# Kernel optimization log

Hardware: AMD Instinct MI355X
Metric: run time of the kernel (lower is better)

The kernel has to match this reference:

```python
import jax, jax.numpy as jnp
import numpy as np


def _make_dplr_hippo(N):
    # Standard HiPPO-LegS -> NPLR -> DPLR construction (Annotated S4).
    p = np.sqrt(1.0 + 2.0 * np.arange(N))
    A = p[:, None] * p[None, :]
    A = np.tril(A) - np.diag(np.arange(N))
    A = -A
    P = np.sqrt(np.arange(N) + 0.5)
    B = np.sqrt(2.0 * np.arange(N) + 1.0)
    # Normal part S = A + P P^T is skew-symmetric + const*I
    S = A + P[:, None] * P[None, :]
    Lambda_real = np.mean(np.diagonal(S)) * np.ones(N)  # = -0.5
    Lambda_imag, V = np.linalg.eigh(S * -1j)            # S*-1j is Hermitian
    Lambda = Lambda_real + 1j * Lambda_imag
    Pc = V.conj().T @ P
    Bc = V.conj().T @ B
    return Lambda, Pc, Bc


N_STATE = 64
SEQ_LEN = 16384
BATCH = 1024


def setup_inputs() -> dict:
    key = jax.random.key(0)
    kx, kcr, kci = jax.random.split(key, 3)
    Lambda, P, B = _make_dplr_hippo(N_STATE)
    scale = 0.5 ** 0.5
    return {
        "x": jax.random.normal(kx, (BATCH, SEQ_LEN), dtype=jnp.float32),
        "Lambda_real": jnp.asarray(Lambda.real, dtype=jnp.float32),
        "Lambda_imag": jnp.asarray(Lambda.imag, dtype=jnp.float32),
        "P_real": jnp.asarray(P.real, dtype=jnp.float32),
        "P_imag": jnp.asarray(P.imag, dtype=jnp.float32),
        "B_real": jnp.asarray(B.real, dtype=jnp.float32),
        "B_imag": jnp.asarray(B.imag, dtype=jnp.float32),
        "C_real": jax.random.normal(kcr, (N_STATE,), dtype=jnp.float32) * scale,
        "C_imag": jax.random.normal(kci, (N_STATE,), dtype=jnp.float32) * scale,
        "step_size": jnp.asarray(0.01, dtype=jnp.float32),
    }


def _s4_fourier_kernel(Lambda, P, Q, B, C, step, L):
    # Evaluate the DPLR SSM generating function at the L roots of unity
    # via 4 Cauchy dot products (the classic S4 bottleneck).
    k = jnp.arange(L, dtype=jnp.float32)
    Omega = jnp.exp(-2j * jnp.pi * k / L)                 # [L] complex64
    g = (2.0 / step) * (1.0 - Omega) / (1.0 + Omega)      # [L]
    c = 2.0 / (1.0 + Omega)                               # [L]
    inv = 1.0 / (g[:, None] - Lambda[None, :])            # [L, N] Cauchy denominators
    a0 = jnp.conj(C)
    a1 = jnp.conj(Q)
    k00 = inv @ (a0 * B)   # [L]
    k01 = inv @ (a0 * P)
    k10 = inv @ (a1 * B)
    k11 = inv @ (a1 * P)
    return c * (k00 - k01 * (1.0 / (1.0 + k11)) * k10)    # [L]


def reference(x, Lambda_real, Lambda_imag, P_real, P_imag, B_real, B_imag,
              C_real, C_imag, step_size):
    L = x.shape[-1]
    Lambda = Lambda_real + 1j * Lambda_imag
    P = P_real + 1j * P_imag
    B = B_real + 1j * B_imag
    C_tilde = C_real + 1j * C_imag
    # Original computes the kernel under torch.no_grad().
    kernel = _s4_fourier_kernel(Lambda, P, P, B, C_tilde, step_size, L)  # [L]
    fft_u = jnp.fft.fft(x, n=L)              # [batch, L] complex64
    y = jnp.fft.ifft(kernel * fft_u, n=L)    # circular conv in freq domain
    return y.real
```

## Files before the change

kernel.cpp:

```cpp
#include <hip/hip_runtime.h>
#include <math.h>

#define LFFT 16384
#define NTHREADS 1024
#define LDS_PITCH 17

#define LDS_FENCE() asm volatile("s_waitcnt lgkmcnt(0)" ::: "memory")

__device__ __forceinline__ float2 cadd(float2 a, float2 b){ return make_float2(a.x+b.x, a.y+b.y); }
__device__ __forceinline__ float2 csub(float2 a, float2 b){ return make_float2(a.x-b.x, a.y-b.y); }
__device__ __forceinline__ float2 cmul(float2 a, float2 b){ return make_float2(a.x*b.x - a.y*b.y, a.x*b.y + a.y*b.x); }

template<int S> __device__ __forceinline__ float2 mul_is(float2 a) {
    return make_float2(-(float)S * a.y, (float)S * a.x);
}

template<int S> __device__ __forceinline__ void dft4_t(float2& a0, float2& a1, float2& a2, float2& a3) {
    float2 t0 = cadd(a0, a2);
    float2 t1 = csub(a0, a2);
    float2 t2 = cadd(a1, a3);
    float2 t3 = csub(a1, a3);
    a0 = cadd(t0, t2);
    a2 = csub(t0, t2);
    const float s = (float)S;
    a1 = make_float2(t1.x - s * t3.y, t1.y + s * t3.x);
    a3 = make_float2(t1.x + s * t3.y, t1.y - s * t3.x);
}

#define C16A 0.92387953251128675613f
#define C16B 0.70710678118654752440f
#define C16C 0.38268343236508977173f

template<int S> __device__ __forceinline__ void dft16_t(float2 r[16]) {
    const float s = (float)S;
    const float2 w1 = make_float2( C16A, s * C16C);
    const float2 w2 = make_float2( C16B, s * C16B);
    const float2 w3 = make_float2( C16C, s * C16A);
    const float2 w6 = make_float2(-C16B, s * C16B);
    const float2 w9 = make_float2(-C16A, -s * C16C);
    float2 g[4][4];
    #pragma unroll
    for (int b = 0; b < 4; ++b) {
        float2 a0 = r[b], a1 = r[b+4], a2 = r[b+8], a3 = r[b+12];
        dft4_t<S>(a0, a1, a2, a3);
        g[b][0] = a0; g[b][1] = a1; g[b][2] = a2; g[b][3] = a3;
    }
    g[1][1] = cmul(g[1][1], w1);  g[1][2] = cmul(g[1][2], w2);  g[1][3] = cmul(g[1][3], w3);
    g[2][1] = cmul(g[2][1], w2);  g[2][2] = mul_is<S>(g[2][2]); g[2][3] = cmul(g[2][3], w6);
    g[3][1] = cmul(g[3][1], w3);  g[3][2] = cmul(g[3][2], w6);  g[3][3] = cmul(g[3][3], w9);
    #pragma unroll
    for (int ka = 0; ka < 4; ++ka) {
        float2 a0 = g[0][ka], a1 = g[1][ka], a2 = g[2][ka], a3 = g[3][ka];
        dft4_t<S>(a0, a1, a2, a3);
        r[ka] = a0; r[ka+4] = a1; r[ka+8] = a2; r[ka+12] = a3;
    }
}

__device__ __forceinline__ void twiddle15(float2 r[16], float2 w) {
    float2 w2 = cmul(w, w);
    float2 we = w2;
    float2 wo = cmul(w, w2);
    r[1] = cmul(r[1], w);
    r[2] = cmul(r[2], we);
    r[3] = cmul(r[3], wo);
    #pragma unroll
    for (int j = 2; j <= 7; ++j) {
        we = cmul(we, w2);  r[2*j]   = cmul(r[2*j],   we);
        wo = cmul(wo, w2);  r[2*j+1] = cmul(r[2*j+1], wo);
    }
}

__global__ void s4_eval(const float* __restrict__ Lr, const float* __restrict__ Li,
                        const float* __restrict__ Pr, const float* __restrict__ Pi,
                        const float* __restrict__ Br, const float* __restrict__ Bi,
                        const float* __restrict__ Cr, const float* __restrict__ Ci,
                        const float* __restrict__ step_ptr,
                        float2* __restrict__ Kraw, float2* __restrict__ twid)
{
    int m = blockIdx.x * blockDim.x + threadIdx.x;
    if (m >= LFFT) return;
    double theta = (-2.0 * M_PI / (double)LFFT) * (double)m;
    double si, co;
    sincos(theta, &si, &co);
    twid[m] = make_float2((float)co, (float)si);

    double step = (double)step_ptr[0];
    double opr = 1.0 + co, opi = si;
    double omr = 1.0 - co, omi = -si;
    double iden = 1.0 / (opr*opr + opi*opi);
    double gs = 2.0 / step;
    double gr = gs * (omr*opr + omi*opi) * iden;
    double gi = gs * (omi*opr - omr*opi) * iden;
    double cr = 2.0 * opr * iden;
    double ci = -2.0 * opi * iden;

    double k00r=0,k00i=0,k01r=0,k01i=0,k10r=0,k10i=0,k11r=0,k11i=0;
    for (int n = 0; n < 64; ++n) {
        double dr = gr - (double)Lr[n];
        double di = gi - (double)Li[n];
        double id2 = 1.0 / (dr*dr + di*di);
        double vr =  dr * id2;
        double vi = -di * id2;
        double a0r = (double)Cr[n], a0i = -(double)Ci[n];
        double a1r = (double)Pr[n], a1i = -(double)Pi[n];
        double br  = (double)Br[n], bi  = (double)Bi[n];
        double pr  = (double)Pr[n], pi  = (double)Pi[n];
        double e00r = a0r*br - a0i*bi, e00i = a0r*bi + a0i*br;
        double e01r = a0r*pr - a0i*pi, e01i = a0r*pi + a0i*pr;
        double e10r = a1r*br - a1i*bi, e10i = a1r*bi + a1i*br;
        double e11r = a1r*pr - a1i*pi, e11i = a1r*pi + a1i*pr;
        k00r += vr*e00r - vi*e00i;  k00i += vr*e00i + vi*e00r;
        k01r += vr*e01r - vi*e01i;  k01i += vr*e01i + vi*e01r;
        k10r += vr*e10r - vi*e10i;  k10i += vr*e10i + vi*e10r;
        k11r += vr*e11r - vi*e11i;  k11i += vr*e11i + vi*e11r;
    }
    double rr = 1.0 + k11r, ri = k11i;
    double ir2 = 1.0 / (rr*rr + ri*ri);
    double qr0 = k01r*k10r - k01i*k10i;
    double qi0 = k01r*k10i + k01i*k10r;
    double qr = (qr0*rr + qi0*ri) * ir2;
    double qi = (qi0*rr - qr0*ri) * ir2;
    double sr = k00r - qr, sim = k00i - qi;
    Kraw[m] = make_float2((float)(cr*sr - ci*sim), (float)(cr*sim + ci*sr));
}

__global__ void s4_perm(const float2* __restrict__ Kraw, float2* __restrict__ Kperm)
{
    int p = blockIdx.x * blockDim.x + threadIdx.x;
    if (p >= LFFT) return;
    int t = p >> 4, j = p & 15;
    int k1 = t >> 6, k3 = (t >> 2) & 15, k5h = t & 3;
    int k5l = j >> 2, k6 = j & 3;
    int m = k1 + 16*k3 + 256*(4*k5h + k5l) + 4096*k6;
    float2 a = Kraw[m];
    float2 b = Kraw[(LFFT - m) & (LFFT - 1)];
    const float s = 0.5f / (float)LFFT;
    Kperm[p] = make_float2(s * (a.x + b.x), s * (a.y - b.y));
}

__global__ __launch_bounds__(NTHREADS, 4) void fft_conv(
    const float* __restrict__ x, float* __restrict__ y,
    const float2* __restrict__ twid, const float2* __restrict__ kperm)
{
    __shared__ float2 lds[NTHREADS * LDS_PITCH];
    const int t    = threadIdx.x;
    const int lane = t & 63;
    const int w    = t >> 6;
    const int l2   = t & 3;
    const int h    = (t >> 2) & 15;
    const size_t rowbase = (size_t)blockIdx.x * 2u * LFFT;
    const float* x0 = x + rowbase;
    const float* x1 = x0 + LFFT;

    float2 r[16];

    #pragma unroll
    for (int a = 0; a < 16; ++a)
        r[a] = make_float2(x0[t + NTHREADS*a], x1[t + NTHREADS*a]);

    dft16_t<-1>(r);
    twiddle15(r, twid[t]);

    #pragma unroll
    for (int k = 0; k < 16; ++k)
        lds[(k*64 + lane) * LDS_PITCH + w] = r[k];
    __syncthreads();
    #pragma unroll
    for (int a = 0; a < 16; ++a)
        r[a] = lds[t * LDS_PITCH + a];
    LDS_FENCE();

    dft16_t<-1>(r);
    twiddle15(r, twid[16 * lane]);

    #pragma unroll
    for (int k = 0; k < 16; ++k)
        lds[(w*64 + 4*k + l2) * LDS_PITCH + h] = r[k];
    LDS_FENCE();
    #pragma unroll
    for (int a = 0; a < 16; ++a)
        r[a] = lds[t * LDS_PITCH + a];
    LDS_FENCE();

    dft16_t<-1>(r);
    twiddle15(r, twid[256 * l2]);

    #pragma unroll
    for (int k = 0; k < 16; ++k)
        lds[((t & ~3) + (k >> 2)) * LDS_PITCH + 4*(k & 3) + l2] = r[k];
    LDS_FENCE();
    #pragma unroll
    for (int j = 0; j < 16; ++j)
        r[j] = lds[t * LDS_PITCH + j];
    LDS_FENCE();

    #pragma unroll
    for (int q = 0; q < 4; ++q)
        dft4_t<-1>(r[4*q], r[4*q+1], r[4*q+2], r[4*q+3]);

    {
        const float4* kp4 = (const float4*)(kperm + t * 16);
        #pragma unroll
        for (int c = 0; c < 2; ++c) {
            float4 kv[4];
            #pragma unroll
            for (int i = 0; i < 4; ++i) kv[i] = kp4[4*c + i];
            #pragma unroll
            for (int i = 0; i < 4; ++i) {
                r[8*c + 2*i]     = cmul(r[8*c + 2*i],     make_float2(kv[i].x, kv[i].y));
                r[8*c + 2*i + 1] = cmul(r[8*c + 2*i + 1], make_float2(kv[i].z, kv[i].w));
            }
        }
    }

    #pragma unroll
    for (int q = 0; q < 4; ++q)
        dft4_t<1>(r[4*q], r[4*q+1], r[4*q+2], r[4*q+3]);

    #pragma unroll
    for (int j = 0; j < 16; ++j)
        lds[((t & ~3) + (j & 3)) * LDS_PITCH + ((4*l2 + (j >> 2)) ^ h)] = r[j];
    LDS_FENCE();
    #pragma unroll
    for (int k = 0; k < 16; ++k)
        r[k] = lds[t * LDS_PITCH + (k ^ h)];
    LDS_FENCE();

    { float2 ww = twid[256 * l2]; twiddle15(r, make_float2(ww.x, -ww.y)); }
    dft16_t<1>(r);

    #pragma unroll
    for (int a = 0; a < 16; ++a)
        lds[(w*64 + l2 + 4*a) * LDS_PITCH + h] = r[a];
    LDS_FENCE();
    #pragma unroll
    for (int k = 0; k < 16; ++k)
        r[k] = lds[t * LDS_PITCH + k];

    { float2 ww = twid[16 * lane]; twiddle15(r, make_float2(ww.x, -ww.y)); }
    dft16_t<1>(r);

    __syncthreads();
    #pragma unroll
    for (int a = 0; a < 16; ++a)
        lds[(lane + 64*a) * LDS_PITCH + w] = r[a];
    __syncthreads();
    #pragma unroll
    for (int k = 0; k < 16; ++k)
        r[k] = lds[t * LDS_PITCH + k];

    { float2 ww = twid[t]; twiddle15(r, make_float2(ww.x, -ww.y)); }
    dft16_t<1>(r);

    float* y0 = y + rowbase;
    float* y1 = y0 + LFFT;
    #pragma unroll
    for (int a = 0; a < 16; ++a) {
        y0[t + NTHREADS*a] = r[a].x;
        y1[t + NTHREADS*a] = r[a].y;
    }
}

extern "C" void kernel_launch(void* const* d_in, const int* in_sizes, int n_in,
                              void* d_out, int out_size, void* d_ws, size_t ws_size,
                              hipStream_t stream)
{
    const float* x  = (const float*)d_in[0];
    const float* Lr = (const float*)d_in[1];
    const float* Li = (const float*)d_in[2];
    const float* Pr = (const float*)d_in[3];
    const float* Pi = (const float*)d_in[4];
    const float* Br = (const float*)d_in[5];
    const float* Bi = (const float*)d_in[6];
    const float* Cr = (const float*)d_in[7];
    const float* Ci = (const float*)d_in[8];
    const float* st = (const float*)d_in[9];

    const int rows = in_sizes[0] / LFFT;

    float2* twid  = (float2*)d_ws;
    float2* Kraw  = twid + LFFT;
    float2* Kperm = Kraw + LFFT;

    s4_eval<<<LFFT / 256, 256, 0, stream>>>(Lr, Li, Pr, Pi, Br, Bi, Cr, Ci, st,
                                            Kraw, twid);
    s4_perm<<<LFFT / 256, 256, 0, stream>>>(Kraw, Kperm);
    fft_conv<<<rows / 2, NTHREADS, 0, stream>>>(x, (float*)d_out, twid, Kperm);
}
```

Before: 74.00 us.

## Replace two-row complex FFT packing with real-FFT via half-length complex transform

Switches from processing two real rows as one 16384-point complex FFT to treating each real row as an 8192-point complex FFT of packed even/odd samples. The kernel spectrum is folded into precomputed U/V coefficients, so the real-to-complex post-processing and the complex-to-real pre-processing collapse into one combination of Z[k] with conj(Z[-k]), read from LDS. Blocks shrink to 512 threads with one row each, and there are three radix-16 stages plus a shuffle-based radix-2. This changes the block count, LDS usage and register pressure, and the pairing step adds extra LDS gathers and barriers.

```diff
diff --git a/kernel.cpp b/kernel.cpp
--- a/kernel.cpp
+++ b/kernel.cpp
@@ -2,14 +2,16 @@
 #include <math.h>
 
 #define LFFT 16384
-#define NTHREADS 1024
-#define LDS_PITCH 17
+#define MFFT 8192
+#define NT   512
+#define PITCH 17
 
 #define LDS_FENCE() asm volatile("s_waitcnt lgkmcnt(0)" ::: "memory")
 
 __device__ __forceinline__ float2 cadd(float2 a, float2 b){ return make_float2(a.x+b.x, a.y+b.y); }
 __device__ __forceinline__ float2 csub(float2 a, float2 b){ return make_float2(a.x-b.x, a.y-b.y); }
 __device__ __forceinline__ float2 cmul(float2 a, float2 b){ return make_float2(a.x*b.x - a.y*b.y, a.x*b.y + a.y*b.x); }
+__device__ __forceinline__ float2 cmulc(float2 a, float2 b){ return make_float2(a.x*b.x + a.y*b.y, a.y*b.x - a.x*b.y); }
 
 template<int S> __device__ __forceinline__ float2 mul_is(float2 a) {
     return make_float2(-(float)S * a.y, (float)S * a.x);
@@ -75,14 +77,19 @@
                         const float* __restrict__ Br, const float* __restrict__ Bi,
                         const float* __restrict__ Cr, const float* __restrict__ Ci,
                         const float* __restrict__ step_ptr,
-                        float2* __restrict__ Kraw, float2* __restrict__ twid)
+                        float2* __restrict__ Kraw, float2* __restrict__ twidM)
 {
     int m = blockIdx.x * blockDim.x + threadIdx.x;
     if (m >= LFFT) return;
+    if (m < MFFT) {
+        double th2 = (-2.0 * M_PI / (double)MFFT) * (double)m;
+        double s2, c2;
+        sincos(th2, &s2, &c2);
+        twidM[m] = make_float2((float)c2, (float)s2);
+    }
     double theta = (-2.0 * M_PI / (double)LFFT) * (double)m;
     double si, co;
     sincos(theta, &si, &co);
-    twid[m] = make_float2((float)co, (float)si);
 
     double step = (double)step_ptr[0];
     double opr = 1.0 + co, opi = si;
@@ -124,141 +131,134 @@
     Kraw[m] = make_float2((float)(cr*sr - ci*sim), (float)(cr*sim + ci*sr));
 }
 
-__global__ void s4_perm(const float2* __restrict__ Kraw, float2* __restrict__ Kperm)
+__global__ void s4_uv(const float2* __restrict__ Kraw, float4* __restrict__ UV)
 {
     int p = blockIdx.x * blockDim.x + threadIdx.x;
-    if (p >= LFFT) return;
+    if (p >= MFFT) return;
     int t = p >> 4, j = p & 15;
-    int k1 = t >> 6, k3 = (t >> 2) & 15, k5h = t & 3;
-    int k5l = j >> 2, k6 = j & 3;
-    int m = k1 + 16*k3 + 256*(4*k5h + k5l) + 4096*k6;
-    float2 a = Kraw[m];
-    float2 b = Kraw[(LFFT - m) & (LFFT - 1)];
-    const float s = 0.5f / (float)LFFT;
-    Kperm[p] = make_float2(s * (a.x + b.x), s * (a.y - b.y));
-}
-
-__global__ __launch_bounds__(NTHREADS, 4) void fft_conv(
+    int k = (t >> 5) | (((t >> 1) & 15) << 4) | (j << 8) | ((t & 1) << 12);
+
+    float2 Ka = Kraw[k];
+    float2 Kb = Kraw[(LFFT - k) & (LFFT - 1)];
+    float2 Kc = Kraw[k + MFFT];
+    float2 Kd = Kraw[MFFT - k];
+    double ar = 0.5 * ((double)Ka.x + (double)Kb.x);
+    double ai = 0.5 * ((double)Ka.y - (double)Kb.y);
+    double br = 0.5 * ((double)Kc.x + (double)Kd.x);
+    double bi = 0.5 * ((double)Kc.y - (double)Kd.y);
+    double Pr = 0.5 * (ar + br), Pi = 0.5 * (ai + bi);
+    double Qr = 0.5 * (ar - br), Qi = 0.5 * (ai - bi);
+    double th = (2.0 * M_PI / (double)LFFT) * (double)k;
+    double sn, cs;
+    sincos(th, &sn, &cs);
+    double inv = 1.0 / (double)MFFT;
+    double Ur = (Pr - sn * Qr) * inv, Ui = (Pi - sn * Qi) * inv;
+    double Vr = (-cs * Qi) * inv,     Vi = ( cs * Qr) * inv;
+    UV[p] = make_float4((float)Ur, (float)Ui, (float)Vr, (float)Vi);
+}
+
+__global__ __launch_bounds__(NT, 4) void fft_conv(
     const float* __restrict__ x, float* __restrict__ y,
-    const float2* __restrict__ twid, const float2* __restrict__ kperm)
-{
-    __shared__ float2 lds[NTHREADS * LDS_PITCH];
-    const int t    = threadIdx.x;
-    const int lane = t & 63;
-    const int w    = t >> 6;
-    const int l2   = t & 3;
-    const int h    = (t >> 2) & 15;
-    const size_t rowbase = (size_t)blockIdx.x * 2u * LFFT;
-    const float* x0 = x + rowbase;
-    const float* x1 = x0 + LFFT;
+    const float2* __restrict__ twidM, const float4* __restrict__ UV)
+{
+    __shared__ float2 lds[NT * PITCH];
+    const int t = threadIdx.x;
+    const int u = t & 31;
+    const int g = t >> 5;
+    const size_t base = (size_t)blockIdx.x * LFFT;
+    const float2* xz = (const float2*)(x + base);
 
     float2 r[16];
-
-    #pragma unroll
-    for (int a = 0; a < 16; ++a)
-        r[a] = make_float2(x0[t + NTHREADS*a], x1[t + NTHREADS*a]);
+    #pragma unroll
+    for (int a = 0; a < 16; ++a) r[a] = xz[t + NT*a];
 
     dft16_t<-1>(r);
-    twiddle15(r, twid[t]);
+    twiddle15(r, twidM[t]);
 
     #pragma unroll
     for (int k = 0; k < 16; ++k)
-        lds[(k*64 + lane) * LDS_PITCH + w] = r[k];
-    __syncthreads();
-    #pragma unroll
-    for (int a = 0; a < 16; ++a)
-        r[a] = lds[t * LDS_PITCH + a];
+        lds[(32*k + u) * PITCH + g] = r[k];
+    __syncthreads();
+    #pragma unroll
+    for (int b = 0; b < 16; ++b) r[b] = lds[t * PITCH + b];
     LDS_FENCE();
 
     dft16_t<-1>(r);
-    twiddle15(r, twid[16 * lane]);
+    twiddle15(r, twidM[16 * u]);
 
     #pragma unroll
     for (int k = 0; k < 16; ++k)
-        lds[(w*64 + 4*k + l2) * LDS_PITCH + h] = r[k];
-    LDS_FENCE();
-    #pragma unroll
-    for (int a = 0; a < 16; ++a)
-        r[a] = lds[t * LDS_PITCH + a];
+        lds[((t & ~31) + 2*k + (t & 1)) * PITCH + (u >> 1)] = r[k];
+    LDS_FENCE();
+    #pragma unroll
+    for (int m = 0; m < 16; ++m) r[m] = lds[t * PITCH + m];
     LDS_FENCE();
 
     dft16_t<-1>(r);
-    twiddle15(r, twid[256 * l2]);
-
-    #pragma unroll
-    for (int k = 0; k < 16; ++k)
-        lds[((t & ~3) + (k >> 2)) * LDS_PITCH + 4*(k & 3) + l2] = r[k];
-    LDS_FENCE();
-    #pragma unroll
-    for (int j = 0; j < 16; ++j)
-        r[j] = lds[t * LDS_PITCH + j];
-    LDS_FENCE();
-
-    #pragma unroll
-    for (int q = 0; q < 4; ++q)
-        dft4_t<-1>(r[4*q], r[4*q+1], r[4*q+2], r[4*q+3]);
-
+    twiddle15(r, twidM[256 * (t & 1)]);
+
+    #pragma unroll
+    for (int j = 0; j < 16; ++j) {
+        float2 o;
+        o.x = __shfl_xor(r[j].x, 1);
+        o.y = __shfl_xor(r[j].y, 1);
+        r[j] = (t & 1) ? csub(o, r[j]) : cadd(r[j], o);
+    }
+
+    #pragma unroll
+    for (int j = 0; j < 16; ++j) lds[t * PITCH + j] = r[j];
+    __syncthreads();
     {
-        const float4* kp4 = (const float4*)(kperm + t * 16);
+        const float4* uv = UV + t * 16;
+        const int kb = g | (((t >> 1) & 15) << 4) | ((t & 1) << 12);
         #pragma unroll
-        for (int c = 0; c < 2; ++c) {
-            float4 kv[4];
-            #pragma unroll
-            for (int i = 0; i < 4; ++i) kv[i] = kp4[4*c + i];
-            #pragma unroll
-            for (int i = 0; i < 4; ++i) {
-                r[8*c + 2*i]     = cmul(r[8*c + 2*i],     make_float2(kv[i].x, kv[i].y));
-                r[8*c + 2*i + 1] = cmul(r[8*c + 2*i + 1], make_float2(kv[i].z, kv[i].w));
-            }
+        for (int j = 0; j < 16; ++j) {
+            int k  = kb + (j << 8);
+            int kp = (MFFT - k) & (MFFT - 1);
+            int tp = ((kp & 15) << 5) | (((kp >> 4) & 15) << 1) | (kp >> 12);
+            int cp = (kp >> 8) & 15;
+            float2 zp = lds[tp * PITCH + cp];
+            float4 c  = uv[j];
+            r[j] = cadd(cmul(make_float2(c.x, c.y), r[j]),
+                        cmulc(make_float2(c.z, c.w), zp));
         }
     }
-
-    #pragma unroll
-    for (int q = 0; q < 4; ++q)
-        dft4_t<1>(r[4*q], r[4*q+1], r[4*q+2], r[4*q+3]);
-
-    #pragma unroll
-    for (int j = 0; j < 16; ++j)
-        lds[((t & ~3) + (j & 3)) * LDS_PITCH + ((4*l2 + (j >> 2)) ^ h)] = r[j];
-    LDS_FENCE();
-    #pragma unroll
-    for (int k = 0; k < 16; ++k)
-        r[k] = lds[t * LDS_PITCH + (k ^ h)];
-    LDS_FENCE();
-
-    { float2 ww = twid[256 * l2]; twiddle15(r, make_float2(ww.x, -ww.y)); }
+    __syncthreads();
+
+    #pragma unroll
+    for (int j = 0; j < 16; ++j) {
+        float2 o;
+        o.x = __shfl_xor(r[j].x, 1);
+        o.y = __shfl_xor(r[j].y, 1);
+        r[j] = (t & 1) ? csub(o, r[j]) : cadd(r[j], o);
+    }
+    { float2 w0 = twidM[256 * (t & 1)]; twiddle15(r, make_float2(w0.x, -w0.y)); }
     dft16_t<1>(r);
 
     #pragma unroll
-    for (int a = 0; a < 16; ++a)
-        lds[(w*64 + l2 + 4*a) * LDS_PITCH + h] = r[a];
-    LDS_FENCE();
-    #pragma unroll
-    for (int k = 0; k < 16; ++k)
-        r[k] = lds[t * LDS_PITCH + k];
-
-    { float2 ww = twid[16 * lane]; twiddle15(r, make_float2(ww.x, -ww.y)); }
+    for (int m = 0; m < 16; ++m)
+        lds[((t & ~31) + (t & 1) + 2*m) * PITCH + (u >> 1)] = r[m];
+    LDS_FENCE();
+    #pragma unroll
+    for (int k = 0; k < 16; ++k) r[k] = lds[t * PITCH + k];
+
+    { float2 w0 = twidM[16 * u]; twiddle15(r, make_float2(w0.x, -w0.y)); }
     dft16_t<1>(r);
 
     __syncthreads();
     #pragma unroll
-    for (int a = 0; a < 16; ++a)
-        lds[(lane + 64*a) * LDS_PITCH + w] = r[a];
-    __syncthreads();
-    #pragma unroll
-    for (int k = 0; k < 16; ++k)
-        r[k] = lds[t * LDS_PITCH + k];
-
-    { float2 ww = twid[t]; twiddle15(r, make_float2(ww.x, -ww.y)); }
+    for (int b = 0; b < 16; ++b)
+        lds[(u + 32*b) * PITCH + g] = r[b];
+    __syncthreads();
+    #pragma unroll
+    for (int k = 0; k < 16; ++k) r[k] = lds[t * PITCH + k];
+
+    { float2 w0 = twidM[t]; twiddle15(r, make_float2(w0.x, -w0.y)); }
     dft16_t<1>(r);
 
-    float* y0 = y + rowbase;
-    float* y1 = y0 + LFFT;
-    #pragma unroll
-    for (int a = 0; a < 16; ++a) {
-        y0[t + NTHREADS*a] = r[a].x;
-        y1[t + NTHREADS*a] = r[a].y;
-    }
+    float2* yz = (float2*)(y + base);
+    #pragma unroll
+    for (int a = 0; a < 16; ++a) yz[t + NT*a] = r[a];
 }
 
 extern "C" void kernel_launch(void* const* d_in, const int* in_sizes, int n_in,
@@ -278,12 +278,12 @@
 
     const int rows = in_sizes[0] / LFFT;
 
-    float2* twid  = (float2*)d_ws;
-    float2* Kraw  = twid + LFFT;
-    float2* Kperm = Kraw + LFFT;
-
-    s4_eval<<<LFFT / 256, 256, 0, stream>>>(Lr, Li, Pr, Pi, Br, Bi, Cr, Ci, st,
-                                            Kraw, twid);
-    s4_perm<<<LFFT / 256, 256, 0, stream>>>(Kraw, Kperm);
-    fft_conv<<<rows / 2, NTHREADS, 0, stream>>>(x, (float*)d_out, twid, Kperm);
-}
+    float2* Kraw  = (float2*)d_ws;
+    float2* twidM = Kraw + LFFT;
+    float4* UV    = (float4*)(twidM + MFFT);
+
+    s4_eval<<<LFFT / 64, 64, 0, stream>>>(Lr, Li, Pr, Pi, Br, Bi, Cr, Ci, st,
+                                          Kraw, twidM);
+    s4_uv<<<MFFT / 64, 64, 0, stream>>>(Kraw, UV);
+    fft_conv<<<rows, NT, 0, stream>>>(x, (float*)d_out, twidM, UV);
+}
```

Result: slower. 77.09 us (+4.2%).

## Swizzle LDS layout for float4 reads and fuse kernel eval with permutation

Applied to the files above, without the earlier changes.

The FFT convolution's shared-memory rows get a pitch of 18 float2 and an XOR swizzle on column bit 3 keyed by row bit 3. Row reads now use 8 float4 loads instead of 16 float2 loads while trying to avoid bank conflicts. The S4 kernel evaluation and permutation are merged into one launch. That launch does twice the double-precision Cauchy evaluations, one per conjugate pair member, instead of reading a staged Kraw buffer. This saves a launch and a global round trip but doubles the FP64 work in that stage, and the larger pitch raises LDS use per block.

```diff
diff --git a/kernel.cpp b/kernel.cpp
--- a/kernel.cpp
+++ b/kernel.cpp
@@ -3,13 +3,17 @@
 
 #define LFFT 16384
 #define NTHREADS 1024
-#define LDS_PITCH 17
+#define PITCH 18
 
 #define LDS_FENCE() asm volatile("s_waitcnt lgkmcnt(0)" ::: "memory")
 
 __device__ __forceinline__ float2 cadd(float2 a, float2 b){ return make_float2(a.x+b.x, a.y+b.y); }
 __device__ __forceinline__ float2 csub(float2 a, float2 b){ return make_float2(a.x-b.x, a.y-b.y); }
 __device__ __forceinline__ float2 cmul(float2 a, float2 b){ return make_float2(a.x*b.x - a.y*b.y, a.x*b.y + a.y*b.x); }
+
+__device__ __forceinline__ int sw(int row, int col) {
+    return row * PITCH + (col ^ (((row >> 3) & 1) << 3));
+}
 
 template<int S> __device__ __forceinline__ float2 mul_is(float2 a) {
     return make_float2(-(float)S * a.y, (float)S * a.x);
@@ -70,21 +74,15 @@
     }
 }
 
-__global__ void s4_eval(const float* __restrict__ Lr, const float* __restrict__ Li,
+__device__ float2 evalK(int m, double step,
+                        const float* __restrict__ Lr, const float* __restrict__ Li,
                         const float* __restrict__ Pr, const float* __restrict__ Pi,
                         const float* __restrict__ Br, const float* __restrict__ Bi,
-                        const float* __restrict__ Cr, const float* __restrict__ Ci,
-                        const float* __restrict__ step_ptr,
-                        float2* __restrict__ Kraw, float2* __restrict__ twid)
+                        const float* __restrict__ Cr, const float* __restrict__ Ci)
 {
-    int m = blockIdx.x * blockDim.x + threadIdx.x;
-    if (m >= LFFT) return;
     double theta = (-2.0 * M_PI / (double)LFFT) * (double)m;
     double si, co;
     sincos(theta, &si, &co);
-    twid[m] = make_float2((float)co, (float)si);
-
-    double step = (double)step_ptr[0];
     double opr = 1.0 + co, opi = si;
     double omr = 1.0 - co, omi = -si;
     double iden = 1.0 / (opr*opr + opi*opi);
@@ -121,33 +119,55 @@
     double qr = (qr0*rr + qi0*ri) * ir2;
     double qi = (qi0*rr - qr0*ri) * ir2;
     double sr = k00r - qr, sim = k00i - qi;
-    Kraw[m] = make_float2((float)(cr*sr - ci*sim), (float)(cr*sim + ci*sr));
-}
-
-__global__ void s4_perm(const float2* __restrict__ Kraw, float2* __restrict__ Kperm)
+    return make_float2((float)(cr*sr - ci*sim), (float)(cr*sim + ci*sr));
+}
+
+__global__ void s4_fused(const float* __restrict__ Lr, const float* __restrict__ Li,
+                         const float* __restrict__ Pr, const float* __restrict__ Pi,
+                         const float* __restrict__ Br, const float* __restrict__ Bi,
+                         const float* __restrict__ Cr, const float* __restrict__ Ci,
+                         const float* __restrict__ step_ptr,
+                         float2* __restrict__ Kperm, float2* __restrict__ twid)
 {
-    int p = blockIdx.x * blockDim.x + threadIdx.x;
-    if (p >= LFFT) return;
-    int t = p >> 4, j = p & 15;
-    int k1 = t >> 6, k3 = (t >> 2) & 15, k5h = t & 3;
-    int k5l = j >> 2, k6 = j & 3;
-    int m = k1 + 16*k3 + 256*(4*k5h + k5l) + 4096*k6;
-    float2 a = Kraw[m];
-    float2 b = Kraw[(LFFT - m) & (LFFT - 1)];
-    const float s = 0.5f / (float)LFFT;
-    Kperm[p] = make_float2(s * (a.x + b.x), s * (a.y - b.y));
+    __shared__ float2 vals[256];
+    const int tid = threadIdx.x;
+    const int T = blockIdx.x * 256 + tid;
+    const int p = T >> 1, c = T & 1;
+
+    int t16 = p >> 4, j = p & 15;
+    int m = (t16 >> 6) + 16 * ((t16 >> 2) & 15)
+          + 256 * (4 * (t16 & 3) + (j >> 2)) + 4096 * (j & 3);
+    int idx = c ? ((LFFT - m) & (LFFT - 1)) : m;
+
+    double step = (double)step_ptr[0];
+    vals[tid] = evalK(idx, step, Lr, Li, Pr, Pi, Br, Bi, Cr, Ci);
+
+    if (c == 0) {
+        double th = (-2.0 * M_PI / (double)LFFT) * (double)p;
+        double si, co;
+        sincos(th, &si, &co);
+        twid[p] = make_float2((float)co, (float)si);
+    }
+    __syncthreads();
+    if (c == 0) {
+        float2 Ka = vals[tid], Kb = vals[tid + 1];
+        const float s = 0.5f / (float)LFFT;
+        Kperm[p] = make_float2(s * (Ka.x + Kb.x), s * (Ka.y - Kb.y));
+    }
 }
 
 __global__ __launch_bounds__(NTHREADS, 4) void fft_conv(
     const float* __restrict__ x, float* __restrict__ y,
     const float2* __restrict__ twid, const float2* __restrict__ kperm)
 {
-    __shared__ float2 lds[NTHREADS * LDS_PITCH];
+    __shared__ float2 lds[NTHREADS * PITCH];
     const int t    = threadIdx.x;
     const int lane = t & 63;
     const int w    = t >> 6;
     const int l2   = t & 3;
     const int h    = (t >> 2) & 15;
+    const int fq   = (t >> 1) & 4;
+    const float4* row4 = (const float4*)(lds + t * PITCH);
     const size_t rowbase = (size_t)blockIdx.x * 2u * LFFT;
     const float* x0 = x + rowbase;
     const float* x1 = x0 + LFFT;
@@ -163,11 +183,14 @@
 
     #pragma unroll
     for (int k = 0; k < 16; ++k)
-        lds[(k*64 + lane) * LDS_PITCH + w] = r[k];
+        lds[sw(k*64 + lane, w)] = r[k];
     __syncthreads();
     #pragma unroll
-    for (int a = 0; a < 16; ++a)
-        r[a] = lds[t * LDS_PITCH + a];
+    for (int q = 0; q < 8; ++q) {
+        float4 v = row4[q ^ fq];
+        r[2*q]   = make_float2(v.x, v.y);
+        r[2*q+1] = make_float2(v.z, v.w);
+    }
     LDS_FENCE();
 
     dft16_t<-1>(r);
@@ -175,11 +198,14 @@
 
     #pragma unroll
     for (int k = 0; k < 16; ++k)
-        lds[(w*64 + 4*k + l2) * LDS_PITCH + h] = r[k];
-    LDS_FENCE();
-    #pragma unroll
-    for (int a = 0; a < 16; ++a)
-        r[a] = lds[t * LDS_PITCH + a];
+        lds[sw(w*64 + 4*k + l2, h)] = r[k];
+    LDS_FENCE();
+    #pragma unroll
+    for (int q = 0; q < 8; ++q) {
+        float4 v = row4[q ^ fq];
+        r[2*q]   = make_float2(v.x, v.y);
+        r[2*q+1] = make_float2(v.z, v.w);
+    }
     LDS_FENCE();
 
     dft16_t<-1>(r);
@@ -187,11 +213,14 @@
 
     #pragma unroll
     for (int k = 0; k < 16; ++k)
-        lds[((t & ~3) + (k >> 2)) * LDS_PITCH + 4*(k & 3) + l2] = r[k];
-    LDS_FENCE();
-    #pragma unroll
-    for (int j = 0; j < 16; ++j)
-        r[j] = lds[t * LDS_PITCH + j];
+        lds[sw((t & ~3) + (k >> 2), 4*(k & 3) + l2)] = r[k];
+    LDS_FENCE();
+    #pragma unroll
+    for (int q = 0; q < 8; ++q) {
+        float4 v = row4[q ^ fq];
+        r[2*q]   = make_float2(v.x, v.y);
+        r[2*q+1] = make_float2(v.z, v.w);
+    }
     LDS_FENCE();
 
     #pragma unroll
@@ -219,11 +248,11 @@
 
     #pragma unroll
     for (int j = 0; j < 16; ++j)
-        lds[((t & ~3) + (j & 3)) * LDS_PITCH + ((4*l2 + (j >> 2)) ^ h)] = r[j];
+        lds[sw((t & ~3) + (j & 3), (4*l2 + (j >> 2)) ^ h)] = r[j];
     LDS_FENCE();
     #pragma unroll
     for (int k = 0; k < 16; ++k)
-        r[k] = lds[t * LDS_PITCH + (k ^ h)];
+        r[k] = lds[sw(t, k ^ h)];
     LDS_FENCE();
 
     { float2 ww = twid[256 * l2]; twiddle15(r, make_float2(ww.x, -ww.y)); }
@@ -231,11 +260,14 @@
 
     #pragma unroll
     for (int a = 0; a < 16; ++a)
-        lds[(w*64 + l2 + 4*a) * LDS_PITCH + h] = r[a];
-    LDS_FENCE();
-    #pragma unroll
-    for (int k = 0; k < 16; ++k)
-        r[k] = lds[t * LDS_PITCH + k];
+        lds[sw(w*64 + l2 + 4*a, h)] = r[a];
+    LDS_FENCE();
+    #pragma unroll
+    for (int q = 0; q < 8; ++q) {
+        float4 v = row4[q ^ fq];
+        r[2*q]   = make_float2(v.x, v.y);
+        r[2*q+1] = make_float2(v.z, v.w);
+    }
 
     { float2 ww = twid[16 * lane]; twiddle15(r, make_float2(ww.x, -ww.y)); }
     dft16_t<1>(r);
@@ -243,11 +275,14 @@
     __syncthreads();
     #pragma unroll
     for (int a = 0; a < 16; ++a)
-        lds[(lane + 64*a) * LDS_PITCH + w] = r[a];
+        lds[sw(lane + 64*a, w)] = r[a];
     __syncthreads();
     #pragma unroll
-    for (int k = 0; k < 16; ++k)
-        r[k] = lds[t * LDS_PITCH + k];
+    for (int q = 0; q < 8; ++q) {
+        float4 v = row4[q ^ fq];
+        r[2*q]   = make_float2(v.x, v.y);
+        r[2*q+1] = make_float2(v.z, v.w);
+    }
 
     { float2 ww = twid[t]; twiddle15(r, make_float2(ww.x, -ww.y)); }
     dft16_t<1>(r);
@@ -279,11 +314,9 @@
     const int rows = in_sizes[0] / LFFT;
 
     float2* twid  = (float2*)d_ws;
-    float2* Kraw  = twid + LFFT;
-    float2* Kperm = Kraw + LFFT;
-
-    s4_eval<<<LFFT / 256, 256, 0, stream>>>(Lr, Li, Pr, Pi, Br, Bi, Cr, Ci, st,
-                                            Kraw, twid);
-    s4_perm<<<LFFT / 256, 256, 0, stream>>>(Kraw, Kperm);
+    float2* Kperm = twid + LFFT;
+
+    s4_fused<<<(2 * LFFT) / 256, 256, 0, stream>>>(Lr, Li, Pr, Pi, Br, Bi,
+                                                   Cr, Ci, st, Kperm, twid);
     fft_conv<<<rows / 2, NTHREADS, 0, stream>>>(x, (float*)d_out, twid, Kperm);
 }
```

New measurement: 77.23 us. 1.04x slower.
